# Performance work log

Measured on AMD Instinct MI355X. Metric: run time of the kernel, lower is better.

## Reference

```python
import jax, jax.numpy as jnp
import numpy as np

M = 16          # max number of instance ids (0 = background)
DELTA_AGG = 0.5
DELTA_DIS = 3.0


def setup_inputs() -> dict:
    key = jax.random.key(0)
    k1, k2 = jax.random.split(key)
    preds = jax.random.normal(k1, (8, 6, 640, 640), dtype=jnp.float32)
    targets = jax.random.randint(k2, (8, 2, 640, 640), 0, M).astype(jnp.int32)
    return {"preds": preds, "targets": targets}


def _seg_sum(vals, ids):
    # vals: [P] or [P, C], ids: [P] -> segment sums with M segments
    return jax.ops.segment_sum(vals, ids, num_segments=M)


def reference(preds, targets):
    N = preds.shape[0]
    sim = preds[:, 2:, :, :].reshape(N, 4, -1).transpose(0, 2, 1)  # N x P x 4
    text = targets[:, 0].reshape(N, -1)                            # N x P
    kern = targets[:, 1].reshape(N, -1)                            # N x P
    P = sim.shape[1]

    seg = jax.vmap(_seg_sum)
    ones = jnp.ones((N, P), sim.dtype)
    cnt_k = seg(ones, kern)                         # N x M kernel pixel counts
    cnt_t = seg(ones, text)                         # N x M text pixel counts
    G = seg(sim, kern) / jnp.maximum(cnt_k, 1.0)[..., None]  # N x M x 4, G_Ki means

    inst = jnp.arange(M)
    valid = (cnt_k > 0) & (cnt_t > 0) & (inst[None, :] >= 1)  # N x M (skip id 0)
    nv = jnp.sum(valid, axis=1)                                # N, number of valid instances

    # ---- aggregation loss: per text pixel, distance to its instance's kernel mean
    G_t = jnp.take_along_axis(G, text[..., None], axis=1)      # N x P x 4
    d = jnp.linalg.norm(sim - G_t, axis=-1) - DELTA_AGG        # N x P
    l = jnp.log(jnp.square(jnp.maximum(d, 0.0)) + 1.0)         # N x P
    l_mean = seg(l, text) / jnp.maximum(cnt_t, 1.0)            # N x M per-instance mean
    agg = jnp.sum(jnp.where(valid, l_mean, 0.0), axis=1) / jnp.maximum(nv, 1)

    # ---- discrimination loss: pairwise distances between valid kernel means
    pair = valid[:, :, None] & valid[:, None, :] & ~jnp.eye(M, dtype=bool)[None]
    sq = jnp.sum(jnp.square(G[:, :, None, :] - G[:, None, :, :]), axis=-1)  # N x M x M
    dist = jnp.sqrt(jnp.where(pair, sq, 1.0))
    lp = jnp.where(pair, jnp.log(jnp.square(jnp.maximum(DELTA_DIS - dist, 0.0)) + 1.0), 0.0)
    dis = jnp.where(nv > 1, 0.5 * jnp.sum(lp, axis=(1, 2)) / jnp.maximum(nv * (nv - 1), 1), 0.0)

    return agg.astype(jnp.float32), dis.astype(jnp.float32)
```

## Files before the change

### kernel.cpp

```cpp
#include <hip/hip_runtime.h>
#include <math.h>

#define NB 8
#define MSEG 16
#define PPIX (640*640)
#define PV4 (PPIX/4)
#define GRIDX 128
#define STRIDE (GRIDX*256)
#define FULLCOV (3*STRIDE)
#define DELTA_AGG 0.5f
#define DELTA_DIS 3.0f

typedef float v2f __attribute__((ext_vector_type(2)));

#define OFF_A1 0
#define OFF_GC (NB*80)
#define OFF_A2 (NB*160)
#define WS_ZERO_FLOATS (NB*192)

__global__ __launch_bounds__(256, 3) void pass1_kernel(
    const float* __restrict__ preds, const int* __restrict__ targets,
    float* __restrict__ ws) {
  const int n = blockIdx.y, blk = blockIdx.x;
  const int tid = threadIdx.x, lane = tid & 63, w = tid >> 6;

  const float4* __restrict__ pc0 = (const float4*)(preds + ((size_t)n*6 + 2)*PPIX);
  const float4* __restrict__ pc1 = (const float4*)(preds + ((size_t)n*6 + 3)*PPIX);
  const float4* __restrict__ pc2 = (const float4*)(preds + ((size_t)n*6 + 4)*PPIX);
  const float4* __restrict__ pc3 = (const float4*)(preds + ((size_t)n*6 + 5)*PPIX);
  const int4*  __restrict__ kernv = (const int4*)(targets + ((size_t)n*2 + 1)*PPIX);

  v2f acc01[MSEG], acc23[MSEG];
  float cntk[MSEG];
#pragma unroll
  for (int m = 0; m < MSEG; ++m) {
    acc01[m] = (v2f){0.f, 0.f}; acc23[m] = (v2f){0.f, 0.f}; cntk[m] = 0.f;
  }

#define PIX1(K, A0, A1, A2, A3) do {                                \
    int k_ = (K);                                                   \
    v2f p01 = {(A0), (A1)}, p23 = {(A2), (A3)};                     \
    _Pragma("unroll")                                               \
    for (int m = 0; m < MSEG; ++m) {                                \
      float fk = (k_ == m) ? 1.0f : 0.0f;                           \
      v2f fk2 = {fk, fk};                                           \
      acc01[m] = __builtin_elementwise_fma(fk2, p01, acc01[m]);     \
      acc23[m] = __builtin_elementwise_fma(fk2, p23, acc23[m]);     \
      cntk[m] += fk;                                                \
    } } while (0)

#define GRP1(KK, VA, VB, VC, VD) do {                \
    PIX1((KK).x, (VA).x, (VB).x, (VC).x, (VD).x);    \
    PIX1((KK).y, (VA).y, (VB).y, (VC).y, (VD).y);    \
    PIX1((KK).z, (VA).z, (VB).z, (VC).z, (VD).z);    \
    PIX1((KK).w, (VA).w, (VB).w, (VC).w, (VD).w);    \
  } while (0)

  const int base = blk*256 + tid;
  int4 kc = kernv[base];
  float4 va = pc0[base], vb = pc1[base], vc = pc2[base], vd = pc3[base];

  {
    const int p = base + STRIDE;
    int4 kn = kernv[p];
    float4 an = pc0[p], bn = pc1[p], cn = pc2[p], dn = pc3[p];
    GRP1(kc, va, vb, vc, vd);
    kc = kn; va = an; vb = bn; vc = cn; vd = dn;
  }
  {
    const int p = base + 2*STRIDE;
    int4 kn = kernv[p];
    float4 an = pc0[p], bn = pc1[p], cn = pc2[p], dn = pc3[p];
    GRP1(kc, va, vb, vc, vd);
    kc = kn; va = an; vb = bn; vc = cn; vd = dn;
  }
  {
    int4 kr; float4 ar, br, cr, dr;
    const int pr = FULLCOV + blk*32 + (tid & 31);
    if (tid < 32) { kr = kernv[pr]; ar = pc0[pr]; br = pc1[pr]; cr = pc2[pr]; dr = pc3[pr]; }
    GRP1(kc, va, vb, vc, vd);
    if (tid < 32) GRP1(kr, ar, br, cr, dr);
  }
#undef GRP1
#undef PIX1

  float acc[80];
#pragma unroll
  for (int m = 0; m < MSEG; ++m) {
    acc[m]      = acc01[m].x;
    acc[16 + m] = acc01[m].y;
    acc[32 + m] = acc23[m].x;
    acc[48 + m] = acc23[m].y;
    acc[64 + m] = cntk[m];
  }

#pragma unroll
  for (int s = 0; s < 6; ++s) {
    const int dist = 32 >> s;
    const bool hi = (lane & dist) != 0;
#pragma unroll
    for (int v = 0; v < (32 >> s); ++v) {
      float keep = hi ? acc[v + (32 >> s)] : acc[v];
      float send = hi ? acc[v] : acc[v + (32 >> s)];
      acc[v] = keep + __shfl_xor(send, dist);
    }
  }
  float cn16[16];
#pragma unroll
  for (int m = 0; m < MSEG; ++m) cn16[m] = acc[64 + m];
#pragma unroll
  for (int s = 0; s < 4; ++s) {
    const int dist = 32 >> s;
    const int half = 8 >> s;
    const bool hi = (lane & dist) != 0;
#pragma unroll
    for (int v = 0; v < half; ++v) {
      float keep = hi ? cn16[v + half] : cn16[v];
      float send = hi ? cn16[v] : cn16[v + half];
      cn16[v] = keep + __shfl_xor(send, dist);
    }
  }
  float ckt = cn16[0];
  ckt += __shfl_xor(ckt, 2);
  ckt += __shfl_xor(ckt, 1);

  __shared__ float s_v[4][64];
  __shared__ float s_c[4][16];
  s_v[w][lane] = acc[0];
  if ((lane & 3) == 0) s_c[w][lane >> 2] = ckt;
  __syncthreads();

  if (tid < 64) {
    atomicAdd(&ws[OFF_A1 + n*80 + tid],
              s_v[0][tid] + s_v[1][tid] + s_v[2][tid] + s_v[3][tid]);
  } else if (tid < 80) {
    int i = tid - 64;
    atomicAdd(&ws[OFF_A1 + n*80 + tid],
              s_c[0][i] + s_c[1][i] + s_c[2][i] + s_c[3][i]);
  }
}

__global__ __launch_bounds__(128) void finalize_G_kernel(float* __restrict__ ws) {
  const int n = blockIdx.x;
  const int tid = threadIdx.x;
  __shared__ float raw[80];
  if (tid < 80) raw[tid] = ws[OFF_A1 + n*80 + tid];
  __syncthreads();
  if (tid < 64) {
    int ch = tid >> 4, m = tid & 15;
    ws[OFF_GC + n*80 + m*4 + ch] = raw[tid] / fmaxf(raw[64 + m], 1.0f);
  } else if (tid < 80) {
    ws[OFF_GC + n*80 + tid] = raw[tid];
  }
}

__global__ __launch_bounds__(256, 4) void pass2_kernel(
    const float* __restrict__ preds, const int* __restrict__ targets,
    float* __restrict__ ws) {
  const int n = blockIdx.y, blk = blockIdx.x;
  const int tid = threadIdx.x, lane = tid & 63, w = tid >> 6;

  const float4* __restrict__ pc0 = (const float4*)(preds + ((size_t)n*6 + 2)*PPIX);
  const float4* __restrict__ pc1 = (const float4*)(preds + ((size_t)n*6 + 3)*PPIX);
  const float4* __restrict__ pc2 = (const float4*)(preds + ((size_t)n*6 + 4)*PPIX);
  const float4* __restrict__ pc3 = (const float4*)(preds + ((size_t)n*6 + 5)*PPIX);
  const int4*  __restrict__ textv = (const int4*)(targets + (size_t)n*2*PPIX);

  __shared__ float4 s_G[MSEG];
  if (tid < MSEG) s_G[tid] = ((const float4*)(ws + OFF_GC + n*80))[tid];

  v2f lc[MSEG];
#pragma unroll
  for (int m = 0; m < MSEG; ++m) lc[m] = (v2f){0.f, 0.f};

  const int base = blk*256 + tid;
  int4 tc = textv[base];
  float4 va = pc0[base], vb = pc1[base], vc = pc2[base], vd = pc3[base];
  __syncthreads();

#define PIX2(T, A0, A1, A2, A3) do {                            \
    int t_ = (T);                                               \
    float4 gv = s_G[t_];                                        \
    float dx = (A0) - gv.x, dy = (A1) - gv.y;                   \
    float dz = (A2) - gv.z, dw = (A3) - gv.w;                   \
    float sq = fmaf(dx, dx, fmaf(dy, dy, fmaf(dz, dz, dw*dw))); \
    float dd = fmaxf(__fsqrt_rn(sq) - DELTA_AGG, 0.f);          \
    float l = __logf(fmaf(dd, dd, 1.f));                        \
    v2f l1 = {l, 1.0f};                                         \
    _Pragma("unroll")                                           \
    for (int m = 0; m < MSEG; ++m) {                            \
      float fk = (t_ == m) ? 1.0f : 0.0f;                       \
      v2f fk2 = {fk, fk};                                       \
      lc[m] = __builtin_elementwise_fma(fk2, l1, lc[m]);        \
    } } while (0)

#define GRP2(TT, VA, VB, VC, VD) do {                \
    PIX2((TT).x, (VA).x, (VB).x, (VC).x, (VD).x);    \
    PIX2((TT).y, (VA).y, (VB).y, (VC).y, (VD).y);    \
    PIX2((TT).z, (VA).z, (VB).z, (VC).z, (VD).z);    \
    PIX2((TT).w, (VA).w, (VB).w, (VC).w, (VD).w);    \
  } while (0)

  {
    const int p = base + STRIDE;
    int4 tn = textv[p];
    float4 an = pc0[p], bn = pc1[p], cn = pc2[p], dn = pc3[p];
    GRP2(tc, va, vb, vc, vd);
    tc = tn; va = an; vb = bn; vc = cn; vd = dn;
  }
  {
    const int p = base + 2*STRIDE;
    int4 tn = textv[p];
    float4 an = pc0[p], bn = pc1[p], cn = pc2[p], dn = pc3[p];
    GRP2(tc, va, vb, vc, vd);
    tc = tn; va = an; vb = bn; vc = cn; vd = dn;
  }
  {
    int4 tr; float4 ar, br, cr, dr;
    const int pr = FULLCOV + blk*32 + (tid & 31);
    if (tid < 32) { tr = textv[pr]; ar = pc0[pr]; br = pc1[pr]; cr = pc2[pr]; dr = pc3[pr]; }
    GRP2(tc, va, vb, vc, vd);
    if (tid < 32) GRP2(tr, ar, br, cr, dr);
  }
#undef GRP2
#undef PIX2

  float ls[MSEG], ct[MSEG];
#pragma unroll
  for (int m = 0; m < MSEG; ++m) { ls[m] = lc[m].x; ct[m] = lc[m].y; }

  float t0, t1;
#pragma unroll
  for (int s = 0; s < 4; ++s) {
    const int dist = 32 >> s; const int half = 8 >> s;
    const bool hi = (lane & dist) != 0;
#pragma unroll
    for (int v = 0; v < half; ++v) {
      float keep = hi ? ls[v + half] : ls[v];
      float send = hi ? ls[v] : ls[v + half];
      ls[v] = keep + __shfl_xor(send, dist);
    }
  }
  t0 = ls[0]; t0 += __shfl_xor(t0, 2); t0 += __shfl_xor(t0, 1);
#pragma unroll
  for (int s = 0; s < 4; ++s) {
    const int dist = 32 >> s; const int half = 8 >> s;
    const bool hi = (lane & dist) != 0;
#pragma unroll
    for (int v = 0; v < half; ++v) {
      float keep = hi ? ct[v + half] : ct[v];
      float send = hi ? ct[v] : ct[v + half];
      ct[v] = keep + __shfl_xor(send, dist);
    }
  }
  t1 = ct[0]; t1 += __shfl_xor(t1, 2); t1 += __shfl_xor(t1, 1);

  __shared__ float s_l[4][16];
  __shared__ float s_t[4][16];
  if ((lane & 3) == 0) { s_l[w][lane >> 2] = t0; s_t[w][lane >> 2] = t1; }
  __syncthreads();

  if (tid < 16)
    atomicAdd(&ws[OFF_A2 + n*32 + tid],
              s_l[0][tid] + s_l[1][tid] + s_l[2][tid] + s_l[3][tid]);
  else if (tid < 32) {
    int i = tid - 16;
    atomicAdd(&ws[OFF_A2 + n*32 + tid],
              s_t[0][i] + s_t[1][i] + s_t[2][i] + s_t[3][i]);
  }
}

__global__ __launch_bounds__(256) void finalize2_kernel(
    const float* __restrict__ ws, float* __restrict__ out) {
  const int n = blockIdx.x;
  const int tid = threadIdx.x;

  __shared__ float s2[32];
  __shared__ float sG[MSEG][4];
  __shared__ float sck[MSEG];
  __shared__ int   sval[MSEG];
  __shared__ int   snv;
  __shared__ float red[256];
  __shared__ float agg_sum;

  if (tid < 32) {
    s2[tid] = ws[OFF_A2 + n*32 + tid];
  } else if (tid >= 32 && tid < 48) {
    sck[tid - 32] = ws[OFF_GC + n*80 + 64 + (tid - 32)];
  } else if (tid >= 64 && tid < 128) {
    int i = tid - 64;
    sG[i >> 2][i & 3] = ws[OFF_GC + n*80 + i];
  }
  __syncthreads();
  if (tid < MSEG)
    sval[tid] = (tid >= 1) && (sck[tid] > 0.f) && (s2[16 + tid] > 0.f);
  __syncthreads();
  if (tid == 0) { int nv = 0; for (int m = 0; m < MSEG; m++) nv += sval[m]; snv = nv; }

  float av = 0.f;
  if (tid < MSEG && sval[tid]) av = s2[tid] / fmaxf(s2[16 + tid], 1.0f);
  red[tid] = av;
  __syncthreads();
  for (int s = 128; s > 0; s >>= 1) {
    if (tid < s) red[tid] += red[tid + s];
    __syncthreads();
  }
  if (tid == 0) agg_sum = red[0];
  __syncthreads();

  float lp = 0.f;
  {
    int i = tid >> 4, j = tid & 15;
    if (i != j && sval[i] && sval[j]) {
      float dx = sG[i][0] - sG[j][0];
      float dy = sG[i][1] - sG[j][1];
      float dz = sG[i][2] - sG[j][2];
      float dw = sG[i][3] - sG[j][3];
      float dist = sqrtf(dx*dx + dy*dy + dz*dz + dw*dw);
      float t = fmaxf(DELTA_DIS - dist, 0.f);
      lp = logf(t*t + 1.f);
    }
  }
  red[tid] = lp;
  __syncthreads();
  for (int s = 128; s > 0; s >>= 1) {
    if (tid < s) red[tid] += red[tid + s];
    __syncthreads();
  }
  if (tid == 0) {
    int nv = snv;
    out[n] = agg_sum / (float)(nv > 1 ? nv : 1);
    out[NB + n] = (nv > 1) ? 0.5f * red[0] / (float)(nv * (nv - 1)) : 0.f;
  }
}

extern "C" void kernel_launch(void* const* d_in, const int* in_sizes, int n_in,
                              void* d_out, int out_size, void* d_ws, size_t ws_size,
                              hipStream_t stream) {
  const float* preds   = (const float*)d_in[0];
  const int*   targets = (const int*)d_in[1];
  float* out = (float*)d_out;
  float* ws  = (float*)d_ws;

  hipMemsetAsync(d_ws, 0, WS_ZERO_FLOATS * sizeof(float), stream);

  dim3 grid(GRIDX, NB);
  pass1_kernel<<<grid, 256, 0, stream>>>(preds, targets, ws);
  finalize_G_kernel<<<NB, 128, 0, stream>>>(ws);
  pass2_kernel<<<grid, 256, 0, stream>>>(preds, targets, ws);
  finalize2_kernel<<<NB, 256, 0, stream>>>(ws, out);
}
```

Measured before the change: 58.79 us.

## Fuse finalize kernels into passes via last-block reduction of per-block partials

Each block now writes its partial sums to its own slot instead of issuing atomics. A per-image counter then selects the last-finishing block, which reduces the partials and runs the finalize step itself. This removes two kernel launches and the atomic contention, at the cost of threadfences and a serialized tail reduction in one block. Pass2 also skips segment 0 in its accumulation loop and its launch bounds change from 4 to 3 blocks per CU.

```diff
diff --git a/kernel.cpp b/kernel.cpp
--- a/kernel.cpp
+++ b/kernel.cpp
@@ -13,14 +13,13 @@
 
 typedef float v2f __attribute__((ext_vector_type(2)));
 
-#define OFF_A1 0
-#define OFF_GC (NB*80)
-#define OFF_A2 (NB*160)
-#define WS_ZERO_FLOATS (NB*192)
+#define OFF_P1 16
+#define OFF_GC (OFF_P1 + NB*80*GRIDX)
+#define OFF_P2 (OFF_GC + NB*80)
 
 __global__ __launch_bounds__(256, 3) void pass1_kernel(
     const float* __restrict__ preds, const int* __restrict__ targets,
-    float* __restrict__ ws) {
+    float* __restrict__ ws, int* __restrict__ ctr) {
   const int n = blockIdx.y, blk = blockIdx.x;
   const int tid = threadIdx.x, lane = tid & 63, w = tid >> 6;
 
@@ -59,7 +58,6 @@
   const int base = blk*256 + tid;
   int4 kc = kernv[base];
   float4 va = pc0[base], vb = pc1[base], vc = pc2[base], vd = pc3[base];
-
   {
     const int p = base + STRIDE;
     int4 kn = kernv[p];
@@ -130,21 +128,33 @@
   if ((lane & 3) == 0) s_c[w][lane >> 2] = ckt;
   __syncthreads();
 
-  if (tid < 64) {
-    atomicAdd(&ws[OFF_A1 + n*80 + tid],
-              s_v[0][tid] + s_v[1][tid] + s_v[2][tid] + s_v[3][tid]);
-  } else if (tid < 80) {
+  if (tid < 64)
+    ws[OFF_P1 + ((size_t)n*80 + tid)*GRIDX + blk] =
+        s_v[0][tid] + s_v[1][tid] + s_v[2][tid] + s_v[3][tid];
+  else if (tid < 80) {
     int i = tid - 64;
-    atomicAdd(&ws[OFF_A1 + n*80 + tid],
-              s_c[0][i] + s_c[1][i] + s_c[2][i] + s_c[3][i]);
-  }
-}
-
-__global__ __launch_bounds__(128) void finalize_G_kernel(float* __restrict__ ws) {
-  const int n = blockIdx.x;
-  const int tid = threadIdx.x;
+    ws[OFF_P1 + ((size_t)n*80 + tid)*GRIDX + blk] =
+        s_c[0][i] + s_c[1][i] + s_c[2][i] + s_c[3][i];
+  }
+
+  __threadfence();
+  __shared__ int s_last;
+  if (tid == 0) s_last = (atomicAdd(&ctr[n], 1) == GRIDX - 1);
+  __syncthreads();
+  if (!s_last) return;
+  __threadfence();
+
   __shared__ float raw[80];
-  if (tid < 80) raw[tid] = ws[OFF_A1 + n*80 + tid];
+  if (tid < 80) {
+    const float4* p4 = (const float4*)(ws + OFF_P1 + ((size_t)n*80 + tid)*GRIDX);
+    float s = 0.f;
+#pragma unroll
+    for (int i = 0; i < GRIDX/4; ++i) {
+      float4 v = p4[i];
+      s += (v.x + v.y) + (v.z + v.w);
+    }
+    raw[tid] = s;
+  }
   __syncthreads();
   if (tid < 64) {
     int ch = tid >> 4, m = tid & 15;
@@ -154,9 +164,9 @@
   }
 }
 
-__global__ __launch_bounds__(256, 4) void pass2_kernel(
+__global__ __launch_bounds__(256, 3) void pass2_kernel(
     const float* __restrict__ preds, const int* __restrict__ targets,
-    float* __restrict__ ws) {
+    float* __restrict__ ws, int* __restrict__ ctr, float* __restrict__ out) {
   const int n = blockIdx.y, blk = blockIdx.x;
   const int tid = threadIdx.x, lane = tid & 63, w = tid >> 6;
 
@@ -188,7 +198,7 @@
     float l = __logf(fmaf(dd, dd, 1.f));                        \
     v2f l1 = {l, 1.0f};                                         \
     _Pragma("unroll")                                           \
-    for (int m = 0; m < MSEG; ++m) {                            \
+    for (int m = 1; m < MSEG; ++m) {                            \
       float fk = (t_ == m) ? 1.0f : 0.0f;                       \
       v2f fk2 = {fk, fk};                                       \
       lc[m] = __builtin_elementwise_fma(fk2, l1, lc[m]);        \
@@ -261,19 +271,20 @@
   __syncthreads();
 
   if (tid < 16)
-    atomicAdd(&ws[OFF_A2 + n*32 + tid],
-              s_l[0][tid] + s_l[1][tid] + s_l[2][tid] + s_l[3][tid]);
+    ws[OFF_P2 + ((size_t)n*32 + tid)*GRIDX + blk] =
+        s_l[0][tid] + s_l[1][tid] + s_l[2][tid] + s_l[3][tid];
   else if (tid < 32) {
     int i = tid - 16;
-    atomicAdd(&ws[OFF_A2 + n*32 + tid],
-              s_t[0][i] + s_t[1][i] + s_t[2][i] + s_t[3][i]);
-  }
-}
-
-__global__ __launch_bounds__(256) void finalize2_kernel(
-    const float* __restrict__ ws, float* __restrict__ out) {
-  const int n = blockIdx.x;
-  const int tid = threadIdx.x;
+    ws[OFF_P2 + ((size_t)n*32 + tid)*GRIDX + blk] =
+        s_t[0][i] + s_t[1][i] + s_t[2][i] + s_t[3][i];
+  }
+
+  __threadfence();
+  __shared__ int s_last;
+  if (tid == 0) s_last = (atomicAdd(&ctr[NB + n], 1) == GRIDX - 1);
+  __syncthreads();
+  if (!s_last) return;
+  __threadfence();
 
   __shared__ float s2[32];
   __shared__ float sG[MSEG][4];
@@ -284,7 +295,14 @@
   __shared__ float agg_sum;
 
   if (tid < 32) {
-    s2[tid] = ws[OFF_A2 + n*32 + tid];
+    const float4* p4 = (const float4*)(ws + OFF_P2 + ((size_t)n*32 + tid)*GRIDX);
+    float s = 0.f;
+#pragma unroll
+    for (int i = 0; i < GRIDX/4; ++i) {
+      float4 v = p4[i];
+      s += (v.x + v.y) + (v.z + v.w);
+    }
+    s2[tid] = s;
   } else if (tid >= 32 && tid < 48) {
     sck[tid - 32] = ws[OFF_GC + n*80 + 64 + (tid - 32)];
   } else if (tid >= 64 && tid < 128) {
@@ -341,12 +359,11 @@
   const int*   targets = (const int*)d_in[1];
   float* out = (float*)d_out;
   float* ws  = (float*)d_ws;
-
-  hipMemsetAsync(d_ws, 0, WS_ZERO_FLOATS * sizeof(float), stream);
+  int*   ctr = (int*)d_ws;
+
+  hipMemsetAsync(d_ws, 0, 64, stream);
 
   dim3 grid(GRIDX, NB);
-  pass1_kernel<<<grid, 256, 0, stream>>>(preds, targets, ws);
-  finalize_G_kernel<<<NB, 128, 0, stream>>>(ws);
-  pass2_kernel<<<grid, 256, 0, stream>>>(preds, targets, ws);
-  finalize2_kernel<<<NB, 256, 0, stream>>>(ws, out);
+  pass1_kernel<<<grid, 256, 0, stream>>>(preds, targets, ws, ctr);
+  pass2_kernel<<<grid, 256, 0, stream>>>(preds, targets, ws, ctr, out);
 }
```

Measured after the change: 234.7 us. 299% more time.
